# Performance work log

Hardware: AMD Instinct MI355X
Metric: run time of the kernel (lower is better)

Reference implementation:

```python
import jax, jax.numpy as jnp
import numpy as np

# PointCNN layer dims
N, NUM_PTS, P, K, DIMS = 32, 2048, 1024, 16, 3
C_IN, C_OUT = 64, 128
C_HALF = C_OUT // 2            # dense lift of raw features
C_MID = C_OUT // 4             # lifted coord features (C_in != 0)
DM = min(int(np.ceil(C_OUT / C_IN)), 4)   # depth multiplier = 2
C_CAT = C_MID + C_HALF         # 96 channels into X-transform matmul
BN_INV = 1.0 / float(np.sqrt(1.0 + 1e-5))  # inference BN, running mean 0 / var 1


def _dense(x, W, b, g, be):
    # Dense = Linear -> ELU -> BatchNorm (inference affine)
    return g * (jax.nn.elu(x @ W + b) * BN_INV) + be


def setup_inputs() -> dict:
    key = jax.random.key(0)
    ks = jax.random.split(key, 24)
    def rn(k, shape, s=0.1):
        return (jax.random.normal(k, shape) * s).astype(jnp.float32)
    return {
        "rep_pts": jax.random.normal(ks[0], (N, P, DIMS), jnp.float32),
        "pts": jax.random.normal(ks[1], (N, NUM_PTS, DIMS), jnp.float32),
        "fts": jax.random.normal(ks[2], (N, NUM_PTS, C_IN), jnp.float32),
        "pts_idx": jax.random.randint(ks[3], (N, P, K), 0, NUM_PTS, dtype=jnp.int32),
        # PointCNN.dense : C_in -> C_out//2
        "d0_W": rn(ks[4], (C_IN, C_HALF)), "d0_b": rn(ks[5], (C_HALF,)),
        "d0_g": jnp.ones((C_HALF,), jnp.float32), "d0_be": rn(ks[6], (C_HALF,)),
        # XConv.dense1 : dims -> C_mid
        "d1_W": rn(ks[7], (DIMS, C_MID)), "d1_b": rn(ks[8], (C_MID,)),
        "d1_g": jnp.ones((C_MID,), jnp.float32), "d1_be": rn(ks[9], (C_MID,)),
        # XConv.dense2 : C_mid -> C_mid
        "d2_W": rn(ks[10], (C_MID, C_MID)), "d2_b": rn(ks[11], (C_MID,)),
        "d2_g": jnp.ones((C_MID,), jnp.float32), "d2_be": rn(ks[12], (C_MID,)),
        # x_trans: Conv2d(dims -> K*K, kernel (1,K)) then 2 Dense (no BN)
        "xc_W": rn(ks[13], (K * K, DIMS, K)), "xc_b": rn(ks[14], (K * K,)),
        "xd1_W": rn(ks[15], (K * K, K * K)), "xd1_b": rn(ks[16], (K * K,)),
        "xd2_W": rn(ks[17], (K * K, K * K)), "xd2_b": rn(ks[18], (K * K,)),
        # end_conv: depthwise (1,K) conv + pointwise conv + ELU + BN
        "dw_W": rn(ks[19], (C_CAT, DM, K)), "dw_b": rn(ks[20], (C_CAT * DM,)),
        "pw_W": rn(ks[21], (C_CAT * DM, C_OUT)), "pw_b": rn(ks[22], (C_OUT,)),
        "end_g": jnp.ones((C_OUT,), jnp.float32), "end_be": rn(ks[23], (C_OUT,)),
    }


def reference(rep_pts, pts, fts, pts_idx, d0_W, d0_b, d0_g, d0_be,
              d1_W, d1_b, d1_g, d1_be, d2_W, d2_b, d2_g, d2_be,
              xc_W, xc_b, xd1_W, xd1_b, xd2_W, xd2_b,
              dw_W, dw_b, pw_W, pw_b, end_g, end_be):
    # lift raw features: Dense C_in -> C_out//2
    fts_l = _dense(fts, d0_W, d0_b, d0_g, d0_be)          # (N, NUM_PTS, C_half)
    # select_region: per-batch irregular neighbor gather
    gather = jax.vmap(lambda a, i: a[i])
    pts_reg = gather(pts, pts_idx)                        # (N,P,K,dims)
    fts_reg = gather(fts_l, pts_idx)                      # (N,P,K,C_half)
    pts_local = pts_reg - rep_pts[:, :, None, :]          # center on rep point
    # lifting MLP on local coordinates
    h = _dense(pts_local, d1_W, d1_b, d1_g, d1_be)
    h = _dense(h, d2_W, d2_b, d2_g, d2_be)                # (N,P,K,C_mid)
    fts_cat = jnp.concatenate([h, fts_reg], axis=-1)      # (N,P,K,C_cat)
    # learned X-transform: Conv2d(dims->K*K, (1,K)) collapses K -> 1, then 2 Dense
    X = jax.nn.elu(jnp.einsum('npkd,qdk->npq', pts_local, xc_W) + xc_b)
    X = jax.nn.elu(X @ xd1_W + xd1_b)
    X = (X @ xd2_W + xd2_b).reshape(pts.shape[0], P, K, K)
    fts_X = jnp.einsum('npij,npjc->npic', X, fts_cat)     # (N,P,K,C_cat)
    # depthwise (groups=C_cat, kernel (1,K)) -> channel layout c*DM+m
    dw = jnp.einsum('npkc,cmk->npcm', fts_X, dw_W)
    dw = dw.reshape(pts.shape[0], P, C_CAT * DM) + dw_b
    # pointwise conv + ELU + inference BN, squeeze collapsed K axis
    out = jax.nn.elu(dw @ pw_W + pw_b)
    return end_g * (out * BN_INV) + end_be                # (N,P,C_out)
```

## Files before the change

### kernel.cpp

```cpp
#include <hip/hip_runtime.h>
#include <math.h>

#define NBATCH 32
#define NUMPT 2048
#define PP 1024
#define MPB 16
#define BN_INV 0.9999950000374996f

typedef __attribute__((ext_vector_type(8))) short short8;
typedef __attribute__((ext_vector_type(4))) float f32x4;

#define MFMA(a,b,c) __builtin_amdgcn_mfma_f32_16x16x32_bf16(a,b,c,0,0,0)

#define FTSL_ELEMS 4194304
#define OFF_D0F  0
#define OFF_XCF  4096
#define OFF_X1F  20480
#define OFF_X2F  86016
#define OFF_D2F  151552
#define OFF_PWF  152576
#define TOT_FRAG 177152

static __device__ __forceinline__ float eluf(float x) {
    return x > 0.0f ? x : (__expf(x) - 1.0f);
}
static __device__ __forceinline__ short f2bf(float x) {
    union { float f; unsigned u; } v; v.f = x;
    unsigned r = v.u + 0x7FFFu + ((v.u >> 16) & 1u);
    return (short)(r >> 16);
}

__global__ __launch_bounds__(256) void k_prep(
    const float* __restrict__ d0W, const float* __restrict__ xcW,
    const float* __restrict__ xd1W, const float* __restrict__ xd2W,
    const float* __restrict__ d2W, const float* __restrict__ pwW,
    short* __restrict__ wf)
{
    int gid = blockIdx.x * 256 + threadIdx.x;
    if (gid >= TOT_FRAG) return;
    float val;
    if (gid < OFF_XCF) {
        int e = gid, j = e & 7, lane = (e >> 3) & 63, t = e >> 9;
        int nb = t % 4, kt = t / 4;
        int nn = nb * 16 + (lane & 15), k = kt * 32 + (lane >> 4) * 8 + j;
        val = d0W[k * 64 + nn];
    } else if (gid < OFF_X1F) {
        int e = gid - OFF_XCF, j = e & 7, lane = (e >> 3) & 63, t = e >> 9;
        int nb = t % 16, kt = t / 16;
        int q = nb * 16 + (lane & 15), kk = kt * 32 + (lane >> 4) * 8 + j;
        val = (kk < 48) ? xcW[(q * 3 + (kk >> 4)) * 16 + (kk & 15)] : 0.0f;
    } else if (gid < OFF_X2F) {
        int e = gid - OFF_X1F, j = e & 7, lane = (e >> 3) & 63, t = e >> 9;
        int nb = t % 16, kt = t / 16;
        int nn = nb * 16 + (lane & 15), k = kt * 32 + (lane >> 4) * 8 + j;
        val = xd1W[k * 256 + nn];
    } else if (gid < OFF_D2F) {
        int e = gid - OFF_X2F, j = e & 7, lane = (e >> 3) & 63, t = e >> 9;
        int nb = t % 16, kt = t / 16;
        int nn = nb * 16 + (lane & 15), k = kt * 32 + (lane >> 4) * 8 + j;
        val = xd2W[k * 256 + nn];
    } else if (gid < OFF_PWF) {
        int e = gid - OFF_D2F, j = e & 7, lane = (e >> 3) & 63, t = e >> 9;
        int nb = t % 2;
        int nn = nb * 16 + (lane & 15), k = (lane >> 4) * 8 + j;
        val = d2W[k * 32 + nn];
    } else {
        int e = gid - OFF_PWF, j = e & 7, lane = (e >> 3) & 63, t = e >> 9;
        int nb = t % 8, kt = t / 8;
        int nn = nb * 16 + (lane & 15), k = kt * 32 + (lane >> 4) * 8 + j;
        val = pwW[k * 128 + nn];
    }
    wf[gid] = f2bf(val);
}

__global__ __launch_bounds__(256) void k_dense0m(
    const float* __restrict__ fts, const short* __restrict__ wf,
    const float* __restrict__ b, const float* __restrict__ g,
    const float* __restrict__ be, short* __restrict__ fl)
{
    __shared__ __align__(16) short sA[4096];
    const int tid = threadIdx.x;
    const long base = (long)blockIdx.x * 64 * 64;
    {
        const int r = tid >> 2, k0 = (tid & 3) * 16;
        #pragma unroll
        for (int i = 0; i < 4; ++i) {
            float4 v = *(const float4*)&fts[base + r * 64 + k0 + i * 4];
            float vv[4] = {v.x, v.y, v.z, v.w};
            #pragma unroll
            for (int u = 0; u < 4; ++u) {
                int k = k0 + i * 4 + u;
                sA[(((k >> 5) * 4 + (r >> 4)) * 64 + ((r & 15) + 16 * ((k >> 3) & 3))) * 8 + (k & 7)] = f2bf(vv[u]);
            }
        }
    }
    __syncthreads();
    const int wave = tid >> 6, lane = tid & 63;
    const int col = lane & 15, quad = lane >> 4;
    const int c = wave * 16 + col;
    const float bb = b[c], gg = g[c], bee = be[c];
    const f32x4 fz = {0.f, 0.f, 0.f, 0.f};
    f32x4 acc[4] = {fz, fz, fz, fz};
    const short8* B = (const short8*)(wf + OFF_D0F);
    #pragma unroll
    for (int kt = 0; kt < 2; ++kt) {
        short8 bfr = B[(kt * 4 + wave) * 64 + lane];
        #pragma unroll
        for (int mt = 0; mt < 4; ++mt) {
            short8 afr = *(const short8*)&sA[((kt * 4 + mt) * 64 + lane) * 8];
            acc[mt] = MFMA(afr, bfr, acc[mt]);
        }
    }
    #pragma unroll
    for (int mt = 0; mt < 4; ++mt) {
        #pragma unroll
        for (int r = 0; r < 4; ++r) {
            long row = (long)blockIdx.x * 64 + mt * 16 + quad * 4 + r;
            fl[row * 64 + c] = f2bf(gg * (eluf(acc[mt][r] + bb) * BN_INV) + bee);
        }
    }
}

__global__ __launch_bounds__(256) void k_xconv(
    const float* __restrict__ rep_pts, const float* __restrict__ pts,
    const int* __restrict__ pts_idx, const short* __restrict__ fl,
    const short* __restrict__ wf,
    const float* __restrict__ d1W, const float* __restrict__ d1b,
    const float* __restrict__ d1g, const float* __restrict__ d1be,
    const float* __restrict__ d2b, const float* __restrict__ d2g,
    const float* __restrict__ d2be,
    const float* __restrict__ xcb, const float* __restrict__ xd1b,
    const float* __restrict__ xd2b,
    const float* __restrict__ dwW, const float* __restrict__ dwb,
    const float* __restrict__ pwb,
    const float* __restrict__ endg, const float* __restrict__ endbe,
    float* __restrict__ out)
{
    __shared__ __align__(16) short s_catF[24576];
    __shared__ __align__(16) short s_big[8192];
    __shared__ __align__(16) short s_X0b[4096];
    __shared__ __align__(16) short s_plF[1024];
    __shared__ float s_pl[768];
    __shared__ float s_d1w[192];

    const int tid = threadIdx.x;
    const int wave = tid >> 6, lane = tid & 63;
    const int col = lane & 15, quad = lane >> 4;
    const int n = blockIdx.x >> 6;
    const int pb = (blockIdx.x & 63) * MPB;
    const long prow0 = (long)n * PP + pb;
    short* s_h1F = s_big;
    short* s_X1 = s_big;
    short* s_X2 = s_big + 4096;
    short* s_dwF = s_X0b;
    const f32x4 fz = {0.f, 0.f, 0.f, 0.f};
    const short8 zz = {0, 0, 0, 0, 0, 0, 0, 0};

    for (int i = 768 + tid; i < 1024; i += 256) s_plF[i] = 0;
    if (tid < 96) s_d1w[tid] = d1W[tid];
    else if (tid < 128) { int cc = tid - 96; s_d1w[96 + cc] = d1b[cc]; s_d1w[128 + cc] = d1g[cc]; s_d1w[160 + cc] = d1be[cc]; }
    const int p0 = tid >> 4, k0 = tid & 15;
    const int idxv = pts_idx[(prow0 + p0) * 16 + k0];
    {
        const float* pp = pts + ((long)n * NUMPT + idxv) * 3;
        const float* rp = rep_pts + (prow0 + p0) * 3;
        #pragma unroll
        for (int d = 0; d < 3; ++d) {
            float v = pp[d] - rp[d];
            s_pl[tid * 3 + d] = v;
            int kk = d * 16 + k0;
            s_plF[((kk >> 5) * 64 + ((kk >> 3) & 3) * 16 + p0) * 8 + (kk & 7)] = f2bf(v);
        }
    }
    __syncthreads();

    short8 gv[8];
    {
        const short8* gp = (const short8*)(fl + ((long)n * NUMPT + idxv) * 64);
        #pragma unroll
        for (int i = 0; i < 8; ++i) gv[i] = gp[i];
    }
    for (int e = tid; e < 8192; e += 256) {
        int row = e >> 5, c1 = e & 31;
        float x0 = s_pl[row * 3], x1 = s_pl[row * 3 + 1], x2 = s_pl[row * 3 + 2];
        float z = s_d1w[96 + c1] + x0 * s_d1w[c1] + x1 * s_d1w[32 + c1] + x2 * s_d1w[64 + c1];
        float v = s_d1w[128 + c1] * (eluf(z) * BN_INV) + s_d1w[160 + c1];
        s_h1F[((row >> 4) * 64 + ((c1 >> 3) & 3) * 16 + (row & 15)) * 8 + (c1 & 7)] = f2bf(v);
    }
    {
        const int kq = k0 >> 3, kj = k0 & 7;
        #pragma unroll
        for (int i = 0; i < 8; ++i) {
            #pragma unroll
            for (int u = 0; u < 8; ++u) {
                int cc = 32 + i * 8 + u;
                s_catF[p0 * 1536 + (((cc >> 4) * 2 + kq) * 16 + (cc & 15)) * 8 + kj] = gv[i][u];
            }
        }
    }
    __syncthreads();

    {
        const short8* B = (const short8*)(wf + OFF_D2F);
        short8 b0 = B[lane], b1 = B[64 + lane];
        short8 a[4];
        #pragma unroll
        for (int mt0 = 0; mt0 < 4; ++mt0)
            a[mt0] = *(const short8*)&s_h1F[((wave * 4 + mt0) * 64 + lane) * 8];
        #pragma unroll
        for (int nb = 0; nb < 2; ++nb) {
            int c2 = nb * 16 + col;
            float bb = d2b[c2], gg = d2g[c2], bee = d2be[c2];
            #pragma unroll
            for (int mt0 = 0; mt0 < 4; ++mt0) {
                int mt = wave * 4 + mt0;
                f32x4 acc = MFMA(a[mt0], nb ? b1 : b0, fz);
                #pragma unroll
                for (int r = 0; r < 4; ++r) {
                    int k = quad * 4 + r;
                    float v = gg * (eluf(acc[r] + bb) * BN_INV) + bee;
                    s_catF[mt * 1536 + ((nb * 2 + (k >> 3)) * 16 + col) * 8 + (k & 7)] = f2bf(v);
                }
            }
        }
    }

    {
        short8 a0 = *(const short8*)&s_plF[lane * 8];
        short8 a1 = *(const short8*)&s_plF[(64 + lane) * 8];
        const short8* B = (const short8*)(wf + OFF_XCF);
        #pragma unroll
        for (int t = 0; t < 4; ++t) {
            int nb = wave * 4 + t;
            f32x4 acc = MFMA(a0, B[nb * 64 + lane], fz);
            acc = MFMA(a1, B[(16 + nb) * 64 + lane], acc);
            int q = nb * 16 + col;
            float bq = xcb[q];
            #pragma unroll
            for (int r = 0; r < 4; ++r) {
                int p = quad * 4 + r;
                float v = eluf(acc[r] + bq);
                s_X0b[((q >> 5) * 64 + ((q >> 3) & 3) * 16 + p) * 8 + (q & 7)] = f2bf(v);
            }
        }
    }
    __syncthreads();

    {
        short8 a[8];
        #pragma unroll
        for (int kt = 0; kt < 8; ++kt)
            a[kt] = *(const short8*)&s_X0b[(kt * 64 + lane) * 8];
        const short8* B = (const short8*)(wf + OFF_X1F);
        #pragma unroll
        for (int t = 0; t < 4; ++t) {
            int nb = wave * 4 + t;
            f32x4 acc = fz;
            #pragma unroll
            for (int kt = 0; kt < 8; ++kt)
                acc = MFMA(a[kt], B[(kt * 16 + nb) * 64 + lane], acc);
            int q = nb * 16 + col;
            float bq = xd1b[q];
            #pragma unroll
            for (int r = 0; r < 4; ++r) {
                int p = quad * 4 + r;
                float v = eluf(acc[r] + bq);
                s_X1[((q >> 5) * 64 + ((q >> 3) & 3) * 16 + p) * 8 + (q & 7)] = f2bf(v);
            }
        }
    }
    __syncthreads();

    {
        short8 a[8];
        #pragma unroll
        for (int kt = 0; kt < 8; ++kt)
            a[kt] = *(const short8*)&s_X1[(kt * 64 + lane) * 8];
        const short8* B = (const short8*)(wf + OFF_X2F);
        #pragma unroll
        for (int t = 0; t < 4; ++t) {
            int nb = wave * 4 + t;
            f32x4 acc = fz;
            #pragma unroll
            for (int kt = 0; kt < 8; ++kt)
                acc = MFMA(a[kt], B[(kt * 16 + nb) * 64 + lane], acc);
            float bq = xd2b[nb * 16 + col];
            #pragma unroll
            for (int r = 0; r < 4; ++r) {
                int p = quad * 4 + r;
                float v = acc[r] + bq;
                s_X2[p * 256 + ((col >> 3) * 16 + nb) * 8 + (col & 7)] = f2bf(v);
            }
        }
    }
    __syncthreads();

    {
        float4 wd0[6], wd1[6]; float2 bdw[6];
        #pragma unroll
        for (int nb = 0; nb < 6; ++nb) {
            int c = nb * 16 + col;
            wd0[nb] = *(const float4*)&dwW[(c * 2 + 0) * 16 + quad * 4];
            wd1[nb] = *(const float4*)&dwW[(c * 2 + 1) * 16 + quad * 4];
            bdw[nb] = *(const float2*)&dwb[c * 2];
        }
        #pragma unroll
        for (int pi = 0; pi < 4; ++pi) {
            int p = wave * 4 + pi;
            short8 afr = zz;
            if (lane < 32) afr = *(const short8*)&s_X2[p * 256 + lane * 8];
            #pragma unroll
            for (int nb = 0; nb < 6; ++nb) {
                short8 bfr = zz;
                if (lane < 32) bfr = *(const short8*)&s_catF[p * 1536 + (nb * 32 + lane) * 8];
                f32x4 acc = MFMA(afr, bfr, fz);
                float q0 = acc[0] * wd0[nb].x + acc[1] * wd0[nb].y + acc[2] * wd0[nb].z + acc[3] * wd0[nb].w;
                float q1 = acc[0] * wd1[nb].x + acc[1] * wd1[nb].y + acc[2] * wd1[nb].z + acc[3] * wd1[nb].w;
                q0 += __shfl_xor(q0, 16); q0 += __shfl_xor(q0, 32);
                q1 += __shfl_xor(q1, 16); q1 += __shfl_xor(q1, 32);
                if (quad == 0) {
                    int c2 = col * 2;
                    int ad = (nb * 64 + (c2 >> 3) * 16 + p) * 8 + (c2 & 7);
                    s_dwF[ad]     = f2bf(q0 + bdw[nb].x);
                    s_dwF[ad + 1] = f2bf(q1 + bdw[nb].y);
                }
            }
        }
    }
    __syncthreads();

    {
        short8 a[6];
        #pragma unroll
        for (int kt = 0; kt < 6; ++kt)
            a[kt] = *(const short8*)&s_dwF[(kt * 64 + lane) * 8];
        const short8* B = (const short8*)(wf + OFF_PWF);
        #pragma unroll
        for (int t = 0; t < 2; ++t) {
            int nb = wave * 2 + t;
            f32x4 acc = fz;
            #pragma unroll
            for (int kt = 0; kt < 6; ++kt)
                acc = MFMA(a[kt], B[(kt * 8 + nb) * 64 + lane], acc);
            int o = nb * 16 + col;
            float bo = pwb[o], go = endg[o], beo = endbe[o];
            #pragma unroll
            for (int r = 0; r < 4; ++r) {
                int p = quad * 4 + r;
                out[(prow0 + p) * 128 + o] = go * (eluf(acc[r] + bo) * BN_INV) + beo;
            }
        }
    }
}

extern "C" void kernel_launch(void* const* d_in, const int* in_sizes, int n_in,
                              void* d_out, int out_size, void* d_ws, size_t ws_size,
                              hipStream_t stream) {
    const float* rep_pts = (const float*)d_in[0];
    const float* pts     = (const float*)d_in[1];
    const float* fts     = (const float*)d_in[2];
    const int*   pts_idx = (const int*)d_in[3];
    const float* d0W = (const float*)d_in[4];
    const float* d0b = (const float*)d_in[5];
    const float* d0g = (const float*)d_in[6];
    const float* d0be = (const float*)d_in[7];
    const float* d1W = (const float*)d_in[8];
    const float* d1b = (const float*)d_in[9];
    const float* d1g = (const float*)d_in[10];
    const float* d1be = (const float*)d_in[11];
    const float* d2W = (const float*)d_in[12];
    const float* d2b = (const float*)d_in[13];
    const float* d2g = (const float*)d_in[14];
    const float* d2be = (const float*)d_in[15];
    const float* xcW = (const float*)d_in[16];
    const float* xcb = (const float*)d_in[17];
    const float* xd1W = (const float*)d_in[18];
    const float* xd1b = (const float*)d_in[19];
    const float* xd2W = (const float*)d_in[20];
    const float* xd2b = (const float*)d_in[21];
    const float* dwW = (const float*)d_in[22];
    const float* dwb = (const float*)d_in[23];
    const float* pwW = (const float*)d_in[24];
    const float* pwb = (const float*)d_in[25];
    const float* endg = (const float*)d_in[26];
    const float* endbe = (const float*)d_in[27];
    float* out = (float*)d_out;

    short* wsS = (short*)d_ws;
    short* fl = wsS;
    short* wf = wsS + FTSL_ELEMS;

    k_prep<<<TOT_FRAG / 256, 256, 0, stream>>>(d0W, xcW, xd1W, xd2W, d2W, pwW, wf);
    k_dense0m<<<(NBATCH * NUMPT) / 64, 256, 0, stream>>>(fts, wf, d0b, d0g, d0be, fl);
    k_xconv<<<NBATCH * (PP / MPB), 256, 0, stream>>>(
        rep_pts, pts, pts_idx, fl, wf,
        d1W, d1b, d1g, d1be, d2b, d2g, d2be,
        xcb, xd1b, xd2b, dwW, dwb, pwb, endg, endbe, out);
}
```

Measured before the change: 209.5 us.

## Pad LDS layouts, vectorize stores, and swap dense0 MFMA operands

Pads the shared-memory tiles (catF stride 1552, 520/264 strides, 66-row h1F) to cut LDS bank conflicts, and switches scalar LDS stores to packed short2/short4/short8 stores. The dense0 kernel now handles 128 rows per block with weights as the A operand, which gives 4-wide vectorized output stores. The dense1 lift is computed in registers from global weights instead of through shared staging, which removes one barrier. Risks are higher register pressure and an index error in the new layouts, though they look consistent.

Result: faster. 197.9 us (-5.5%).

```diff
diff --git a/kernel.cpp b/kernel.cpp
--- a/kernel.cpp
+++ b/kernel.cpp
@@ -8,6 +8,8 @@
 #define BN_INV 0.9999950000374996f
 
 typedef __attribute__((ext_vector_type(8))) short short8;
+typedef __attribute__((ext_vector_type(4))) short short4v;
+typedef __attribute__((ext_vector_type(2))) short short2v;
 typedef __attribute__((ext_vector_type(4))) float f32x4;
 
 #define MFMA(a,b,c) __builtin_amdgcn_mfma_f32_16x16x32_bf16(a,b,c,0,0,0)
@@ -20,6 +22,8 @@
 #define OFF_D2F  151552
 #define OFF_PWF  152576
 #define TOT_FRAG 177152
+
+#define CATP 1552
 
 static __device__ __forceinline__ float eluf(float x) {
     return x > 0.0f ? x : (__expf(x) - 1.0f);
@@ -78,45 +82,56 @@
     const float* __restrict__ b, const float* __restrict__ g,
     const float* __restrict__ be, short* __restrict__ fl)
 {
-    __shared__ __align__(16) short sA[4096];
+    __shared__ __align__(16) short sB[2 * 4160];
     const int tid = threadIdx.x;
-    const long base = (long)blockIdx.x * 64 * 64;
-    {
-        const int r = tid >> 2, k0 = (tid & 3) * 16;
-        #pragma unroll
-        for (int i = 0; i < 4; ++i) {
-            float4 v = *(const float4*)&fts[base + r * 64 + k0 + i * 4];
-            float vv[4] = {v.x, v.y, v.z, v.w};
-            #pragma unroll
-            for (int u = 0; u < 4; ++u) {
-                int k = k0 + i * 4 + u;
-                sA[(((k >> 5) * 4 + (r >> 4)) * 64 + ((r & 15) + 16 * ((k >> 3) & 3))) * 8 + (k & 7)] = f2bf(vv[u]);
-            }
-        }
-    }
-    __syncthreads();
+    const long base = (long)blockIdx.x * 128 * 64;
+
+    #pragma unroll
+    for (int it = 0; it < 4; ++it) {
+        const int gidx = tid + it * 256;
+        const int r = gidx >> 3, o = gidx & 7;
+        float4 va = *(const float4*)&fts[base + r * 64 + o * 8];
+        float4 vb = *(const float4*)&fts[base + r * 64 + o * 8 + 4];
+        short8 pk;
+        pk[0] = f2bf(va.x); pk[1] = f2bf(va.y); pk[2] = f2bf(va.z); pk[3] = f2bf(va.w);
+        pk[4] = f2bf(vb.x); pk[5] = f2bf(vb.y); pk[6] = f2bf(vb.z); pk[7] = f2bf(vb.w);
+        *(short8*)&sB[(o >> 2) * 4160 + (r >> 4) * 520 + ((o & 3) * 16 + (r & 15)) * 8] = pk;
+    }
+    __syncthreads();
+
     const int wave = tid >> 6, lane = tid & 63;
     const int col = lane & 15, quad = lane >> 4;
-    const int c = wave * 16 + col;
-    const float bb = b[c], gg = g[c], bee = be[c];
     const f32x4 fz = {0.f, 0.f, 0.f, 0.f};
-    f32x4 acc[4] = {fz, fz, fz, fz};
-    const short8* B = (const short8*)(wf + OFF_D0F);
+    f32x4 acc[2][4] = {{fz, fz, fz, fz}, {fz, fz, fz, fz}};
+    const short8* WA = (const short8*)(wf + OFF_D0F);
     #pragma unroll
     for (int kt = 0; kt < 2; ++kt) {
-        short8 bfr = B[(kt * 4 + wave) * 64 + lane];
-        #pragma unroll
-        for (int mt = 0; mt < 4; ++mt) {
-            short8 afr = *(const short8*)&sA[((kt * 4 + mt) * 64 + lane) * 8];
-            acc[mt] = MFMA(afr, bfr, acc[mt]);
+        short8 af[4];
+        #pragma unroll
+        for (int mt = 0; mt < 4; ++mt) af[mt] = WA[(kt * 4 + mt) * 64 + lane];
+        #pragma unroll
+        for (int ni = 0; ni < 2; ++ni) {
+            short8 bf_ = *(const short8*)&sB[kt * 4160 + (wave * 2 + ni) * 520 + lane * 8];
+            #pragma unroll
+            for (int mt = 0; mt < 4; ++mt)
+                acc[ni][mt] = MFMA(af[mt], bf_, acc[ni][mt]);
         }
     }
     #pragma unroll
     for (int mt = 0; mt < 4; ++mt) {
-        #pragma unroll
-        for (int r = 0; r < 4; ++r) {
-            long row = (long)blockIdx.x * 64 + mt * 16 + quad * 4 + r;
-            fl[row * 64 + c] = f2bf(gg * (eluf(acc[mt][r] + bb) * BN_INV) + bee);
+        const int c0 = mt * 16 + quad * 4;
+        float4 b4 = *(const float4*)&b[c0];
+        float4 g4 = *(const float4*)&g[c0];
+        float4 e4 = *(const float4*)&be[c0];
+        #pragma unroll
+        for (int ni = 0; ni < 2; ++ni) {
+            long rowg = (long)blockIdx.x * 128 + (wave * 2 + ni) * 16 + col;
+            short4v sv;
+            sv[0] = f2bf(g4.x * (eluf(acc[ni][mt][0] + b4.x) * BN_INV) + e4.x);
+            sv[1] = f2bf(g4.y * (eluf(acc[ni][mt][1] + b4.y) * BN_INV) + e4.y);
+            sv[2] = f2bf(g4.z * (eluf(acc[ni][mt][2] + b4.z) * BN_INV) + e4.z);
+            sv[3] = f2bf(g4.w * (eluf(acc[ni][mt][3] + b4.w) * BN_INV) + e4.w);
+            *(short4v*)&fl[rowg * 64 + c0] = sv;
         }
     }
 }
@@ -136,12 +151,10 @@
     const float* __restrict__ endg, const float* __restrict__ endbe,
     float* __restrict__ out)
 {
-    __shared__ __align__(16) short s_catF[24576];
-    __shared__ __align__(16) short s_big[8192];
-    __shared__ __align__(16) short s_X0b[4096];
+    __shared__ __align__(16) short s_catF[MPB * CATP];
+    __shared__ __align__(16) short s_big[8448];
+    __shared__ __align__(16) short s_X0b[4160];
     __shared__ __align__(16) short s_plF[1024];
-    __shared__ float s_pl[768];
-    __shared__ float s_d1w[192];
 
     const int tid = threadIdx.x;
     const int wave = tid >> 6, lane = tid & 63;
@@ -151,28 +164,26 @@
     const long prow0 = (long)n * PP + pb;
     short* s_h1F = s_big;
     short* s_X1 = s_big;
-    short* s_X2 = s_big + 4096;
+    short* s_X2 = s_big + 4160;
     short* s_dwF = s_X0b;
     const f32x4 fz = {0.f, 0.f, 0.f, 0.f};
     const short8 zz = {0, 0, 0, 0, 0, 0, 0, 0};
 
     for (int i = 768 + tid; i < 1024; i += 256) s_plF[i] = 0;
-    if (tid < 96) s_d1w[tid] = d1W[tid];
-    else if (tid < 128) { int cc = tid - 96; s_d1w[96 + cc] = d1b[cc]; s_d1w[128 + cc] = d1g[cc]; s_d1w[160 + cc] = d1be[cc]; }
     const int p0 = tid >> 4, k0 = tid & 15;
     const int idxv = pts_idx[(prow0 + p0) * 16 + k0];
+    float x0, x1, x2;
     {
         const float* pp = pts + ((long)n * NUMPT + idxv) * 3;
         const float* rp = rep_pts + (prow0 + p0) * 3;
+        x0 = pp[0] - rp[0]; x1 = pp[1] - rp[1]; x2 = pp[2] - rp[2];
+        const float v[3] = {x0, x1, x2};
         #pragma unroll
         for (int d = 0; d < 3; ++d) {
-            float v = pp[d] - rp[d];
-            s_pl[tid * 3 + d] = v;
             int kk = d * 16 + k0;
-            s_plF[((kk >> 5) * 64 + ((kk >> 3) & 3) * 16 + p0) * 8 + (kk & 7)] = f2bf(v);
-        }
-    }
-    __syncthreads();
+            s_plF[((kk >> 5) * 64 + ((kk >> 3) & 3) * 16 + p0) * 8 + (kk & 7)] = f2bf(v[d]);
+        }
+    }
 
     short8 gv[8];
     {
@@ -180,22 +191,26 @@
         #pragma unroll
         for (int i = 0; i < 8; ++i) gv[i] = gp[i];
     }
-    for (int e = tid; e < 8192; e += 256) {
-        int row = e >> 5, c1 = e & 31;
-        float x0 = s_pl[row * 3], x1 = s_pl[row * 3 + 1], x2 = s_pl[row * 3 + 2];
-        float z = s_d1w[96 + c1] + x0 * s_d1w[c1] + x1 * s_d1w[32 + c1] + x2 * s_d1w[64 + c1];
-        float v = s_d1w[128 + c1] * (eluf(z) * BN_INV) + s_d1w[160 + c1];
-        s_h1F[((row >> 4) * 64 + ((c1 >> 3) & 3) * 16 + (row & 15)) * 8 + (c1 & 7)] = f2bf(v);
-    }
-    {
-        const int kq = k0 >> 3, kj = k0 & 7;
+
+    #pragma unroll
+    for (int oct = 0; oct < 4; ++oct) {
+        short8 v8;
+        #pragma unroll
+        for (int u = 0; u < 8; ++u) {
+            int c = oct * 8 + u;
+            float z = d1b[c] + x0 * d1W[c] + x1 * d1W[32 + c] + x2 * d1W[64 + c];
+            v8[u] = f2bf(d1g[c] * (eluf(z) * BN_INV) + d1be[c]);
+        }
+        *(short8*)&s_h1F[(p0 * 66 + oct * 16 + k0) * 8] = v8;
+    }
+
+    {
+        const int gbase = p0 * CATP + 32 * 16 + k0;
         #pragma unroll
         for (int i = 0; i < 8; ++i) {
             #pragma unroll
-            for (int u = 0; u < 8; ++u) {
-                int cc = 32 + i * 8 + u;
-                s_catF[p0 * 1536 + (((cc >> 4) * 2 + kq) * 16 + (cc & 15)) * 8 + kj] = gv[i][u];
-            }
+            for (int u = 0; u < 8; ++u)
+                s_catF[gbase + (i * 8 + u) * 16] = gv[i][u];
         }
     }
     __syncthreads();
@@ -206,7 +221,7 @@
         short8 a[4];
         #pragma unroll
         for (int mt0 = 0; mt0 < 4; ++mt0)
-            a[mt0] = *(const short8*)&s_h1F[((wave * 4 + mt0) * 64 + lane) * 8];
+            a[mt0] = *(const short8*)&s_h1F[((wave * 4 + mt0) * 66 + lane) * 8];
         #pragma unroll
         for (int nb = 0; nb < 2; ++nb) {
             int c2 = nb * 16 + col;
@@ -215,12 +230,11 @@
             for (int mt0 = 0; mt0 < 4; ++mt0) {
                 int mt = wave * 4 + mt0;
                 f32x4 acc = MFMA(a[mt0], nb ? b1 : b0, fz);
+                short4v sv;
                 #pragma unroll
-                for (int r = 0; r < 4; ++r) {
-                    int k = quad * 4 + r;
-                    float v = gg * (eluf(acc[r] + bb) * BN_INV) + bee;
-                    s_catF[mt * 1536 + ((nb * 2 + (k >> 3)) * 16 + col) * 8 + (k & 7)] = f2bf(v);
-                }
+                for (int r = 0; r < 4; ++r)
+                    sv[r] = f2bf(gg * (eluf(acc[r] + bb) * BN_INV) + bee);
+                *(short4v*)&s_catF[mt * CATP + c2 * 16 + quad * 4] = sv;
             }
         }
     }
@@ -239,8 +253,8 @@
             #pragma unroll
             for (int r = 0; r < 4; ++r) {
                 int p = quad * 4 + r;
-                float v = eluf(acc[r] + bq);
-                s_X0b[((q >> 5) * 64 + ((q >> 3) & 3) * 16 + p) * 8 + (q & 7)] = f2bf(v);
+                s_X0b[(q >> 5) * 520 + (((q >> 3) & 3) * 16 + p) * 8 + (q & 7)]
+                    = f2bf(eluf(acc[r] + bq));
             }
         }
     }
@@ -250,7 +264,7 @@
         short8 a[8];
         #pragma unroll
         for (int kt = 0; kt < 8; ++kt)
-            a[kt] = *(const short8*)&s_X0b[(kt * 64 + lane) * 8];
+            a[kt] = *(const short8*)&s_X0b[kt * 520 + lane * 8];
         const short8* B = (const short8*)(wf + OFF_X1F);
         #pragma unroll
         for (int t = 0; t < 4; ++t) {
@@ -264,8 +278,8 @@
             #pragma unroll
             for (int r = 0; r < 4; ++r) {
                 int p = quad * 4 + r;
-                float v = eluf(acc[r] + bq);
-                s_X1[((q >> 5) * 64 + ((q >> 3) & 3) * 16 + p) * 8 + (q & 7)] = f2bf(v);
+                s_X1[(q >> 5) * 520 + (((q >> 3) & 3) * 16 + p) * 8 + (q & 7)]
+                    = f2bf(eluf(acc[r] + bq));
             }
         }
     }
@@ -275,7 +289,7 @@
         short8 a[8];
         #pragma unroll
         for (int kt = 0; kt < 8; ++kt)
-            a[kt] = *(const short8*)&s_X1[(kt * 64 + lane) * 8];
+            a[kt] = *(const short8*)&s_X1[kt * 520 + lane * 8];
         const short8* B = (const short8*)(wf + OFF_X2F);
         #pragma unroll
         for (int t = 0; t < 4; ++t) {
@@ -288,8 +302,7 @@
             #pragma unroll
             for (int r = 0; r < 4; ++r) {
                 int p = quad * 4 + r;
-                float v = acc[r] + bq;
-                s_X2[p * 256 + ((col >> 3) * 16 + nb) * 8 + (col & 7)] = f2bf(v);
+                s_X2[p * 264 + ((col >> 3) * 16 + nb) * 8 + (col & 7)] = f2bf(acc[r] + bq);
             }
         }
     }
@@ -308,11 +321,12 @@
         for (int pi = 0; pi < 4; ++pi) {
             int p = wave * 4 + pi;
             short8 afr = zz;
-            if (lane < 32) afr = *(const short8*)&s_X2[p * 256 + lane * 8];
+            if (lane < 32) afr = *(const short8*)&s_X2[p * 264 + lane * 8];
             #pragma unroll
             for (int nb = 0; nb < 6; ++nb) {
                 short8 bfr = zz;
-                if (lane < 32) bfr = *(const short8*)&s_catF[p * 1536 + (nb * 32 + lane) * 8];
+                if (lane < 32)
+                    bfr = *(const short8*)&s_catF[p * CATP + (nb * 16 + col) * 16 + quad * 8];
                 f32x4 acc = MFMA(afr, bfr, fz);
                 float q0 = acc[0] * wd0[nb].x + acc[1] * wd0[nb].y + acc[2] * wd0[nb].z + acc[3] * wd0[nb].w;
                 float q1 = acc[0] * wd1[nb].x + acc[1] * wd1[nb].y + acc[2] * wd1[nb].z + acc[3] * wd1[nb].w;
@@ -321,8 +335,10 @@
                 if (quad == 0) {
                     int c2 = col * 2;
                     int ad = (nb * 64 + (c2 >> 3) * 16 + p) * 8 + (c2 & 7);
-                    s_dwF[ad]     = f2bf(q0 + bdw[nb].x);
-                    s_dwF[ad + 1] = f2bf(q1 + bdw[nb].y);
+                    short2v sv2;
+                    sv2[0] = f2bf(q0 + bdw[nb].x);
+                    sv2[1] = f2bf(q1 + bdw[nb].y);
+                    *(short2v*)&s_dwF[ad] = sv2;
                 }
             }
         }
@@ -390,8 +406,8 @@
     short* fl = wsS;
     short* wf = wsS + FTSL_ELEMS;
 
-    k_prep<<<TOT_FRAG / 256, 256, 0, stream>>>(d0W, xcW, xd1W, xd2W, d2W, pwW, wf);
-    k_dense0m<<<(NBATCH * NUMPT) / 64, 256, 0, stream>>>(fts, wf, d0b, d0g, d0be, fl);
+    k_prep<<<(TOT_FRAG + 255) / 256, 256, 0, stream>>>(d0W, xcW, xd1W, xd2W, d2W, pwW, wf);
+    k_dense0m<<<(NBATCH * NUMPT) / 128, 256, 0, stream>>>(fts, wf, d0b, d0g, d0be, fl);
     k_xconv<<<NBATCH * (PP / MPB), 256, 0, stream>>>(
         rep_pts, pts, pts_idx, fl, wf,
         d1W, d1b, d1g, d1be, d2b, d2g, d2be,
```
